# Kernel optimization log

Measured on AMD Instinct MI355X. Metric: run time of the kernel, lower is better.

## Reference

```python
import jax, jax.numpy as jnp
import numpy as np

B, N = 4, 2048

def setup_inputs() -> dict:
    key = jax.random.key(0)
    k1, k2, k3, k4 = jax.random.split(key, 4)
    return {
        "xyz": jax.random.normal(k1, (B, N, 3), dtype=jnp.float32),
        "scales": jax.random.uniform(k2, (B, N, 3), dtype=jnp.float32),
        "rotations": jax.random.normal(k3, (B, N, 4), dtype=jnp.float32),
        "velocities": jax.random.normal(k4, (B, N, 3), dtype=jnp.float32),
    }

def _quat_to_rotmat(q):
    # q: (B, N, 4) -> (B, N, 3, 3), same formula as the torch module (no normalization)
    qw, qx, qy, qz = q[..., 0], q[..., 1], q[..., 2], q[..., 3]
    R = jnp.stack([
        1 - 2 * qy**2 - 2 * qz**2, 2 * qx * qy - 2 * qz * qw, 2 * qx * qz + 2 * qy * qw,
        2 * qx * qy + 2 * qz * qw, 1 - 2 * qx**2 - 2 * qz**2, 2 * qy * qz - 2 * qx * qw,
        2 * qx * qz - 2 * qy * qw, 2 * qy * qz + 2 * qx * qw, 1 - 2 * qx**2 - 2 * qy**2,
    ], axis=-1)
    return R.reshape(q.shape[0], q.shape[1], 3, 3)

def reference(xyz, scales, rotations, velocities):
    b, n, _ = xyz.shape
    diff = xyz[:, :, None, :] - xyz[:, None, :, :]          # (B,N,N,3)
    dist = jnp.sqrt(jnp.sum(diff * diff, axis=-1) + 1e-8)    # (B,N,N)
    direction = diff / dist[..., None]                        # (B,N,N,3)

    R = _quat_to_rotmat(rotations)                            # (B,N,3,3)
    u_R = jnp.einsum('bnmi,bnij->bnmj', direction, R)         # (B,N,N,3)
    u_R_S = u_R * scales[:, None, :, :]                       # scale of gaussian m
    r_directional = jnp.sqrt(jnp.sum(u_R_S * u_R_S, axis=-1))  # (B,N,N)
    r_total = r_directional + jnp.swapaxes(r_directional, 1, 2)

    overlap = jax.nn.relu(r_total - dist)                     # (B,N,N)
    spectral_repulsion = overlap**2 / (1 + 0.1 * overlap)

    v_rel = velocities[:, :, None, :] - velocities[:, None, :, :]
    v_approach = jnp.sum(v_rel * direction, axis=-1)          # (B,N,N)
    mskd_loss = jnp.sum(overlap * jax.nn.relu(-v_approach)) / (b * n * n)

    mask = jnp.eye(n, dtype=bool)[None]                       # zero self-pairs
    spectral_repulsion = jnp.where(mask, 0.0, spectral_repulsion)
    return jnp.mean(spectral_repulsion) + 0.1 * mskd_loss
```

## Files before the change

### kernel.cpp

```cpp
#include <hip/hip_runtime.h>

#define BB 4
#define NN 2048
#define TS 128
#define T_TILES (NN / TS)
#define NPAIRS (T_TILES * (T_TILES + 1) / 2)
#define MSPLIT 2
#define MH (TS / MSPLIT)
#define MT (MH / 2)
#define JOBS_PER_B (NPAIRS * MSPLIT)
#define NJOBS (JOBS_PER_B * BB)
#define BLK 256
#define SCALE (2.0f / ((float)BB * (float)NN * (float)NN))

__device__ __forceinline__ void quat_to_R(float qw, float qx, float qy, float qz, float* R) {
    R[0] = 1.f - 2.f * (qy * qy + qz * qz);
    R[1] = 2.f * (qx * qy - qz * qw);
    R[2] = 2.f * (qx * qz + qy * qw);
    R[3] = 2.f * (qx * qy + qz * qw);
    R[4] = 1.f - 2.f * (qx * qx + qz * qz);
    R[5] = 2.f * (qy * qz - qx * qw);
    R[6] = 2.f * (qx * qz - qy * qw);
    R[7] = 2.f * (qy * qz + qx * qw);
    R[8] = 1.f - 2.f * (qx * qx + qy * qy);
}

template <bool ATOMIC>
__global__ __launch_bounds__(BLK) void pair_kernel(
    const float* __restrict__ xyz, const float* __restrict__ scales,
    const float* __restrict__ rot, const float* __restrict__ vel,
    float* __restrict__ partials, unsigned int* __restrict__ counter,
    float* __restrict__ outp)
{
    __shared__ float4 sm[MH][5];
    __shared__ float wsum[BLK / 64];
    __shared__ int lastflag;

    const int tid = threadIdx.x;
    const int jid = blockIdx.x;
    const int b   = jid / JOBS_PER_B;
    const int rem = jid % JOBS_PER_B;
    const int p   = rem >> 1;
    const int mh  = rem & 1;

    int ti = (int)((sqrtf(8.f * (float)p + 1.f) - 1.f) * 0.5f);
    while ((ti + 1) * (ti + 2) / 2 <= p) ++ti;
    while (ti * (ti + 1) / 2 > p) --ti;
    const int tj = p - ti * (ti + 1) / 2;
    const bool diag = (ti == tj);

    const int row   = tid & (TS - 1);
    const int msub  = tid >> 7;
    const int n     = ti * TS + row;
    const int m_blk = tj * TS + mh * MH;

    if (tid < MH) {
        const int m = m_blk + tid;
        const size_t i3 = ((size_t)b * NN + m) * 3;
        const size_t i4 = ((size_t)b * NN + m) * 4;
        const float4 q = *reinterpret_cast<const float4*>(rot + i4);
        float R[9];
        quat_to_R(q.x, q.y, q.z, q.w, R);
        sm[tid][0] = make_float4(xyz[i3], xyz[i3 + 1], xyz[i3 + 2], scales[i3]);
        sm[tid][1] = make_float4(scales[i3 + 1], scales[i3 + 2], vel[i3], vel[i3 + 1]);
        sm[tid][2] = make_float4(vel[i3 + 2], R[0], R[1], R[2]);
        sm[tid][3] = make_float4(R[3], R[4], R[5], R[6]);
        sm[tid][4] = make_float4(R[7], R[8], 0.f, 0.f);
    }

    const size_t i3 = ((size_t)b * NN + n) * 3;
    const size_t i4 = ((size_t)b * NN + n) * 4;
    const float px = xyz[i3], py = xyz[i3 + 1], pz = xyz[i3 + 2];
    const float sx = scales[i3], sy = scales[i3 + 1], sz = scales[i3 + 2];
    const float vx = vel[i3], vy = vel[i3 + 1], vz = vel[i3 + 2];
    const float4 qn = *reinterpret_cast<const float4*>(rot + i4);
    float Rn[9];
    quat_to_R(qn.x, qn.y, qn.z, qn.w, Rn);

    __syncthreads();

    float acc = 0.f;
    const int jbase = msub * MT;

    auto inner = [&](bool isDiag) {
        #pragma unroll 4
        for (int jj = 0; jj < MT; ++jj) {
            const int j = jbase + jj;
            const float4 c0 = sm[j][0];
            const float4 c1 = sm[j][1];
            const float4 c2 = sm[j][2];
            const float4 c3 = sm[j][3];
            const float4 c4 = sm[j][4];
            const float dx = px - c0.x, dy = py - c0.y, dz = pz - c0.z;
            const float d2 = fmaf(dx, dx, fmaf(dy, dy, fmaf(dz, dz, 1e-8f)));
            const float rinv = __builtin_amdgcn_rsqf(d2);
            const float a0 = fmaf(dx, Rn[0], fmaf(dy, Rn[3], dz * Rn[6])) * c0.w;
            const float a1 = fmaf(dx, Rn[1], fmaf(dy, Rn[4], dz * Rn[7])) * c1.x;
            const float a2 = fmaf(dx, Rn[2], fmaf(dy, Rn[5], dz * Rn[8])) * c1.y;
            const float qa = __builtin_amdgcn_sqrtf(fmaf(a0, a0, fmaf(a1, a1, a2 * a2)));
            const float b0 = fmaf(dx, c2.y, fmaf(dy, c3.x, dz * c3.w)) * sx;
            const float b1 = fmaf(dx, c2.z, fmaf(dy, c3.y, dz * c4.x)) * sy;
            const float b2 = fmaf(dx, c2.w, fmaf(dy, c3.z, dz * c4.y)) * sz;
            const float qb = __builtin_amdgcn_sqrtf(fmaf(b0, b0, fmaf(b1, b1, b2 * b2)));
            const float w  = fmaxf(qa + qb - d2, 0.f);
            const float ov = w * rinv;
            const float rc = __builtin_amdgcn_rcpf(fmaf(0.1f, ov, 1.f));
            const float vdot = fmaf(vx - c1.z, dx, fmaf(vy - c1.w, dy, (vz - c2.x) * dz));
            const float ramp = fmaxf(-vdot * rinv, 0.f);
            float t = ov * fmaf(ov, rc, 0.1f * ramp);
            if (isDiag && !(m_blk + j < n)) t = 0.f;
            acc += t;
        }
    };
    if (diag) inner(true); else inner(false);

    #pragma unroll
    for (int off = 32; off > 0; off >>= 1)
        acc += __shfl_down(acc, off, 64);
    if ((tid & 63) == 0) wsum[tid >> 6] = acc;
    __syncthreads();

    if (ATOMIC) {
        if (tid == 0) atomicAdd(outp, (wsum[0] + wsum[1] + wsum[2] + wsum[3]) * SCALE);
        return;
    }

    if (tid == 0) {
        const float tot = wsum[0] + wsum[1] + wsum[2] + wsum[3];
        partials[jid] = tot;
        __threadfence();
        const unsigned int done = atomicAdd(counter, 1u);
        lastflag = (done == (unsigned int)(NJOBS - 1));
    }
    __syncthreads();

    if (lastflag && tid < 64) {
        __threadfence();
        const float4* p4 = reinterpret_cast<const float4*>(partials);
        float s = 0.f;
        #pragma unroll
        for (int i = tid; i < NJOBS / 4; i += 64) {
            const float4 v = p4[i];
            s += v.x + v.y + v.z + v.w;
        }
        #pragma unroll
        for (int off = 32; off > 0; off >>= 1)
            s += __shfl_down(s, off, 64);
        if (tid == 0) outp[0] = s * SCALE;
    }
}

extern "C" void kernel_launch(void* const* d_in, const int* in_sizes, int n_in,
                              void* d_out, int out_size, void* d_ws, size_t ws_size,
                              hipStream_t stream)
{
    const float* xyz    = (const float*)d_in[0];
    const float* scales = (const float*)d_in[1];
    const float* rot    = (const float*)d_in[2];
    const float* vel    = (const float*)d_in[3];
    float* out = (float*)d_out;

    if (ws_size >= 256 + NJOBS * sizeof(float)) {
        unsigned int* counter = (unsigned int*)d_ws;
        float* partials = (float*)((char*)d_ws + 256);
        hipMemsetAsync(counter, 0, sizeof(unsigned int), stream);
        pair_kernel<false><<<NJOBS, BLK, 0, stream>>>(xyz, scales, rot, vel,
                                                      partials, counter, out);
    } else {
        hipMemsetAsync(d_out, 0, sizeof(float), stream);
        pair_kernel<true><<<NJOBS, BLK, 0, stream>>>(xyz, scales, rot, vel,
                                                     nullptr, nullptr, out);
    }
}
```

Measured before the change: 35.13 us.

## Register-block four rows per thread and retile into 256x32 pair jobs

Each thread now holds the per-point data of four n rows in registers and evaluates each shared-memory m column against all four, so each LDS read of a column is reused across four pairs. The tile size grows to 256 and the m range is split into 32-wide chunks, with each wave taking 8 columns, which changes the job count and the per-block shape. Launch bounds request four blocks per SM. The cost targeted is LDS traffic per pair; the price is higher register pressure from the four rows' rotation matrices, which could limit occupancy or spill.

```diff
diff --git a/kernel.cpp b/kernel.cpp
--- a/kernel.cpp
+++ b/kernel.cpp
@@ -2,15 +2,16 @@
 
 #define BB 4
 #define NN 2048
-#define TS 128
-#define T_TILES (NN / TS)
-#define NPAIRS (T_TILES * (T_TILES + 1) / 2)
-#define MSPLIT 2
-#define MH (TS / MSPLIT)
-#define MT (MH / 2)
-#define JOBS_PER_B (NPAIRS * MSPLIT)
+#define TS 256
+#define TT (NN / TS)
+#define NPAIRS (TT * (TT + 1) / 2)
+#define MC 32
+#define MSPL (TS / MC)
+#define JOBS_PER_B (NPAIRS * MSPL)
 #define NJOBS (JOBS_PER_B * BB)
 #define BLK 256
+#define ROWS 4
+#define MPW (MC / 4)
 #define SCALE (2.0f / ((float)BB * (float)NN * (float)NN))
 
 __device__ __forceinline__ void quat_to_R(float qw, float qx, float qy, float qz, float* R) {
@@ -26,35 +27,34 @@
 }
 
 template <bool ATOMIC>
-__global__ __launch_bounds__(BLK) void pair_kernel(
+__global__ __launch_bounds__(BLK, 4) void pair_kernel(
     const float* __restrict__ xyz, const float* __restrict__ scales,
     const float* __restrict__ rot, const float* __restrict__ vel,
     float* __restrict__ partials, unsigned int* __restrict__ counter,
     float* __restrict__ outp)
 {
-    __shared__ float4 sm[MH][5];
+    __shared__ float4 sm[MC][5];
     __shared__ float wsum[BLK / 64];
     __shared__ int lastflag;
 
-    const int tid = threadIdx.x;
-    const int jid = blockIdx.x;
-    const int b   = jid / JOBS_PER_B;
-    const int rem = jid % JOBS_PER_B;
-    const int p   = rem >> 1;
-    const int mh  = rem & 1;
+    const int tid  = threadIdx.x;
+    const int lane = tid & 63;
+    const int w    = tid >> 6;
+    const int jid  = blockIdx.x;
+    const int b    = jid / JOBS_PER_B;
+    const int rem  = jid % JOBS_PER_B;
+    const int p    = rem / MSPL;
+    const int mc   = rem % MSPL;
 
-    int ti = (int)((sqrtf(8.f * (float)p + 1.f) - 1.f) * 0.5f);
+    int ti = 0;
     while ((ti + 1) * (ti + 2) / 2 <= p) ++ti;
-    while (ti * (ti + 1) / 2 > p) --ti;
     const int tj = p - ti * (ti + 1) / 2;
     const bool diag = (ti == tj);
 
-    const int row   = tid & (TS - 1);
-    const int msub  = tid >> 7;
-    const int n     = ti * TS + row;
-    const int m_blk = tj * TS + mh * MH;
+    const int n_base = ti * TS;
+    const int m_blk  = tj * TS + mc * MC;
 
-    if (tid < MH) {
+    if (tid < MC) {
         const int m = m_blk + tid;
         const size_t i3 = ((size_t)b * NN + m) * 3;
         const size_t i4 = ((size_t)b * NN + m) * 4;
@@ -68,48 +68,62 @@
         sm[tid][4] = make_float4(R[7], R[8], 0.f, 0.f);
     }
 
-    const size_t i3 = ((size_t)b * NN + n) * 3;
-    const size_t i4 = ((size_t)b * NN + n) * 4;
-    const float px = xyz[i3], py = xyz[i3 + 1], pz = xyz[i3 + 2];
-    const float sx = scales[i3], sy = scales[i3 + 1], sz = scales[i3 + 2];
-    const float vx = vel[i3], vy = vel[i3 + 1], vz = vel[i3 + 2];
-    const float4 qn = *reinterpret_cast<const float4*>(rot + i4);
-    float Rn[9];
-    quat_to_R(qn.x, qn.y, qn.z, qn.w, Rn);
+    float px[ROWS], py[ROWS], pz[ROWS];
+    float sx[ROWS], sy[ROWS], sz[ROWS];
+    float vx[ROWS], vy[ROWS], vz[ROWS];
+    float Rn[ROWS][9];
+    int   nidx[ROWS];
+    #pragma unroll
+    for (int r = 0; r < ROWS; ++r) {
+        const int n = n_base + lane + 64 * r;
+        nidx[r] = n;
+        const size_t i3 = ((size_t)b * NN + n) * 3;
+        const size_t i4 = ((size_t)b * NN + n) * 4;
+        px[r] = xyz[i3]; py[r] = xyz[i3 + 1]; pz[r] = xyz[i3 + 2];
+        sx[r] = scales[i3]; sy[r] = scales[i3 + 1]; sz[r] = scales[i3 + 2];
+        vx[r] = vel[i3]; vy[r] = vel[i3 + 1]; vz[r] = vel[i3 + 2];
+        const float4 q = *reinterpret_cast<const float4*>(rot + i4);
+        quat_to_R(q.x, q.y, q.z, q.w, Rn[r]);
+    }
 
     __syncthreads();
 
     float acc = 0.f;
-    const int jbase = msub * MT;
+    const int jb = w * MPW;
 
     auto inner = [&](bool isDiag) {
-        #pragma unroll 4
-        for (int jj = 0; jj < MT; ++jj) {
-            const int j = jbase + jj;
+        #pragma unroll 2
+        for (int jj = 0; jj < MPW; ++jj) {
+            const int j = jb + jj;
+            const int m = m_blk + j;
             const float4 c0 = sm[j][0];
             const float4 c1 = sm[j][1];
             const float4 c2 = sm[j][2];
             const float4 c3 = sm[j][3];
             const float4 c4 = sm[j][4];
-            const float dx = px - c0.x, dy = py - c0.y, dz = pz - c0.z;
-            const float d2 = fmaf(dx, dx, fmaf(dy, dy, fmaf(dz, dz, 1e-8f)));
-            const float rinv = __builtin_amdgcn_rsqf(d2);
-            const float a0 = fmaf(dx, Rn[0], fmaf(dy, Rn[3], dz * Rn[6])) * c0.w;
-            const float a1 = fmaf(dx, Rn[1], fmaf(dy, Rn[4], dz * Rn[7])) * c1.x;
-            const float a2 = fmaf(dx, Rn[2], fmaf(dy, Rn[5], dz * Rn[8])) * c1.y;
-            const float qa = __builtin_amdgcn_sqrtf(fmaf(a0, a0, fmaf(a1, a1, a2 * a2)));
-            const float b0 = fmaf(dx, c2.y, fmaf(dy, c3.x, dz * c3.w)) * sx;
-            const float b1 = fmaf(dx, c2.z, fmaf(dy, c3.y, dz * c4.x)) * sy;
-            const float b2 = fmaf(dx, c2.w, fmaf(dy, c3.z, dz * c4.y)) * sz;
-            const float qb = __builtin_amdgcn_sqrtf(fmaf(b0, b0, fmaf(b1, b1, b2 * b2)));
-            const float w  = fmaxf(qa + qb - d2, 0.f);
-            const float ov = w * rinv;
-            const float rc = __builtin_amdgcn_rcpf(fmaf(0.1f, ov, 1.f));
-            const float vdot = fmaf(vx - c1.z, dx, fmaf(vy - c1.w, dy, (vz - c2.x) * dz));
-            const float ramp = fmaxf(-vdot * rinv, 0.f);
-            float t = ov * fmaf(ov, rc, 0.1f * ramp);
-            if (isDiag && !(m_blk + j < n)) t = 0.f;
-            acc += t;
+            #pragma unroll
+            for (int r = 0; r < ROWS; ++r) {
+                const float dx = px[r] - c0.x, dy = py[r] - c0.y, dz = pz[r] - c0.z;
+                const float d2 = fmaf(dx, dx, fmaf(dy, dy, fmaf(dz, dz, 1e-8f)));
+                const float rinv = __builtin_amdgcn_rsqf(d2);
+                const float a0 = fmaf(dx, Rn[r][0], fmaf(dy, Rn[r][3], dz * Rn[r][6])) * c0.w;
+                const float a1 = fmaf(dx, Rn[r][1], fmaf(dy, Rn[r][4], dz * Rn[r][7])) * c1.x;
+                const float a2 = fmaf(dx, Rn[r][2], fmaf(dy, Rn[r][5], dz * Rn[r][8])) * c1.y;
+                const float qa = __builtin_amdgcn_sqrtf(fmaf(a0, a0, fmaf(a1, a1, a2 * a2)));
+                const float b0 = fmaf(dx, c2.y, fmaf(dy, c3.x, dz * c3.w)) * sx[r];
+                const float b1 = fmaf(dx, c2.z, fmaf(dy, c3.y, dz * c4.x)) * sy[r];
+                const float b2 = fmaf(dx, c2.w, fmaf(dy, c3.z, dz * c4.y)) * sz[r];
+                const float qb = __builtin_amdgcn_sqrtf(fmaf(b0, b0, fmaf(b1, b1, b2 * b2)));
+                const float ww = fmaxf(qa + qb - d2, 0.f);
+                const float ov = ww * rinv;
+                const float rc = __builtin_amdgcn_rcpf(fmaf(0.1f, ov, 1.f));
+                const float vdot = fmaf(vx[r] - c1.z, dx,
+                                   fmaf(vy[r] - c1.w, dy, (vz[r] - c2.x) * dz));
+                const float ramp = fmaxf(-vdot * rinv, 0.f);
+                float t = ov * fmaf(ov, rc, 0.1f * ramp);
+                if (isDiag && !(m < nidx[r])) t = 0.f;
+                acc += t;
+            }
         }
     };
     if (diag) inner(true); else inner(false);
@@ -117,7 +131,7 @@
     #pragma unroll
     for (int off = 32; off > 0; off >>= 1)
         acc += __shfl_down(acc, off, 64);
-    if ((tid & 63) == 0) wsum[tid >> 6] = acc;
+    if (lane == 0) wsum[w] = acc;
     __syncthreads();
 
     if (ATOMIC) {
@@ -138,7 +152,6 @@
         __threadfence();
         const float4* p4 = reinterpret_cast<const float4*>(partials);
         float s = 0.f;
-        #pragma unroll
         for (int i = tid; i < NJOBS / 4; i += 64) {
             const float4 v = p4[i];
             s += v.x + v.y + v.z + v.w;
```

After: 38.45 us. +9.4%, slower.
